# Kernel tuning notes

Hardware: AMD Instinct MI355X
Metric: run time of the kernel (lower is better)

## Reference

```python
import jax, jax.numpy as jnp
import numpy as np

B, N_IN, N_OUT, DEG = 128, 16384, 8192, 64
N_EDGES = N_OUT * DEG


def setup_inputs() -> dict:
    key = jax.random.key(0)
    k_x, k_src, k_dst, k_w = jax.random.split(key, 4)
    x = jax.random.normal(k_x, (B, N_IN), dtype=jnp.float32)
    # Ragged connectivity flattened to a CSR-like edge list:
    # edge_src[e] -> input feature index, edge_dst[e] -> output unit index.
    edge_src = jax.random.randint(k_src, (N_EDGES,), 0, N_IN, dtype=jnp.int64)
    edge_dst = jnp.sort(jax.random.randint(k_dst, (N_EDGES,), 0, N_OUT, dtype=jnp.int64))
    w = jax.random.normal(k_w, (N_EDGES,), dtype=jnp.float32) * 0.05  # one weight per edge
    bias = jnp.zeros((N_OUT,), dtype=jnp.float32)
    return {"x": x, "w": w, "bias": bias, "edge_src": edge_src, "edge_dst": edge_dst}


def reference(x, w, bias, edge_src, edge_dst):
    # Equivalent to: for each output j, y[:, j] = relu(x[:, edges_j] @ w_j + bias[j])
    # Vectorized as a single gather + weighted scatter-add over the flat edge list.
    n_out = bias.shape[0]
    gathered = x[:, edge_src] * w  # [B, E]
    y = jnp.zeros((x.shape[0], n_out), dtype=x.dtype).at[:, edge_dst].add(gathered)
    return jax.nn.relu(y + bias)
```

## Files before the change

### kernel.cpp

```cpp
#include <hip/hip_runtime.h>
#include <hip/hip_fp16.h>

#define B_DIM   128
#define N_IN    16384
#define N_OUT   8192
#define N_EDGES (N_OUT * 64)

#define J_BLK    8
#define THREADS  (J_BLK * 64)
#define JGROUPS  (N_OUT / J_BLK)

__device__ __forceinline__ int lower_bound_dev(const int* __restrict__ a, int n, int v) {
    int lo = 0, hi = n;
    while (lo < hi) {
        int mid = (lo + hi) >> 1;
        if (a[mid] < v) lo = mid + 1; else hi = mid;
    }
    return lo;
}

__global__ void build_rowptr_kernel(const int* __restrict__ dst, int* __restrict__ rp) {
    const int e = blockIdx.x * blockDim.x + threadIdx.x;
    if (e >= N_EDGES) return;
    const int d     = __builtin_nontemporal_load(dst + e);
    const int dprev = (e == 0) ? -1 : __builtin_nontemporal_load(dst + e - 1);
    for (int j = dprev + 1; j <= d; ++j) rp[j] = e;
    if (e == N_EDGES - 1)
        for (int j = d + 1; j <= N_OUT; ++j) rp[j] = N_EDGES;
}

__global__ __launch_bounds__(256) void transpose_h_kernel(const float* __restrict__ x,
                                                          __half* __restrict__ xTh) {
    __shared__ float tile[64][33];
    const int i0 = blockIdx.x * 32;
    const int b0 = blockIdx.y * 64;
    const int tx = threadIdx.x;
    const int ty = threadIdx.y;
#pragma unroll
    for (int r = 0; r < 64; r += 8)
        tile[ty + r][tx] = __builtin_nontemporal_load(&x[(size_t)(b0 + ty + r) * N_IN + (i0 + tx)]);
    __syncthreads();
    __half2* out = (__half2*)xTh;
#pragma unroll
    for (int rr = 0; rr < 4; ++rr) {
        const int il = rr * 8 + ty;
        const float a = tile[2 * tx][il];
        const float b = tile[2 * tx + 1][il];
        out[(size_t)(i0 + il) * (B_DIM / 2) + (b0 >> 1) + tx] = __floats2half2_rn(a, b);
    }
}

__global__ __launch_bounds__(THREADS, 8) void sparse_layer_h(
        const __half* __restrict__ xTh, const float* __restrict__ w,
        const float* __restrict__ bias, const int* __restrict__ src,
        const int* __restrict__ rp, float* __restrict__ y) {
    __shared__ float tile[J_BLK][132];

    const int tid  = threadIdx.x;
    const int wid  = tid >> 6;
    const int lane = tid & 63;
    const int slot = lane >> 4;
    const int bl   = lane & 15;
    const int j0   = blockIdx.x * J_BLK;
    const int j    = j0 + wid;

    const int e0 = __builtin_amdgcn_readfirstlane(rp[j]);
    const int e1 = __builtin_amdgcn_readfirstlane(rp[j + 1]);

    float acc[8] = {0.f, 0.f, 0.f, 0.f, 0.f, 0.f, 0.f, 0.f};
    const char* xbase = (const char*)xTh + bl * 16;

#pragma unroll 4
    for (int e = e0; e < e1; e += 4) {
        const int  ee    = e + slot;
        const bool valid = ee < e1;
        const int  ec    = valid ? ee : e0;
        const int  s     = __builtin_nontemporal_load(src + ec);
        const float wt   = valid ? __builtin_nontemporal_load(w + ec) : 0.f;
        const float4 raw = *(const float4*)(xbase + (size_t)s * (B_DIM * 2));
        const __half2* hp = (const __half2*)&raw;
#pragma unroll
        for (int q = 0; q < 4; ++q) {
            const float2 f = __half22float2(hp[q]);
            acc[2 * q]     = fmaf(f.x, wt, acc[2 * q]);
            acc[2 * q + 1] = fmaf(f.y, wt, acc[2 * q + 1]);
        }
    }

#pragma unroll
    for (int m = 16; m <= 32; m <<= 1)
#pragma unroll
        for (int q = 0; q < 8; ++q) acc[q] += __shfl_xor(acc[q], m, 64);

    if (slot == 0) {
#pragma unroll
        for (int q = 0; q < 8; ++q) tile[wid][8 * bl + q] = acc[q];
    }
    __syncthreads();

#pragma unroll
    for (int i = tid; i < B_DIM * J_BLK; i += THREADS) {
        const int bb = i >> 3;
        const int jj = i & (J_BLK - 1);
        const float v = tile[jj][bb] + bias[j0 + jj];
        __builtin_nontemporal_store(fmaxf(v, 0.f), &y[(size_t)bb * N_OUT + (j0 + jj)]);
    }
}

__global__ __launch_bounds__(THREADS) void sparse_layer_fallback(
        const float* __restrict__ x, const float* __restrict__ w,
        const float* __restrict__ bias, const int* __restrict__ src,
        const int* __restrict__ dst, float* __restrict__ y) {
    __shared__ float tile[J_BLK][130];
    __shared__ int   srp[J_BLK + 1];

    const int tid  = threadIdx.x;
    const int wid  = tid >> 6;
    const int lane = tid & 63;
    const int j0   = blockIdx.x * J_BLK;

    if (tid <= J_BLK) srp[tid] = lower_bound_dev(dst, N_EDGES, j0 + tid);
    __syncthreads();

    const int e0 = srp[wid], e1 = srp[wid + 1];
    const int b0 = lane * 2;
    float acc0 = 0.f, acc1 = 0.f;
    for (int e = e0; e < e1; ++e) {
        const int   s  = src[e];
        const float wt = w[e];
        acc0 = fmaf(x[(size_t)b0 * N_IN + s], wt, acc0);
        acc1 = fmaf(x[(size_t)(b0 + 1) * N_IN + s], wt, acc1);
    }
    tile[wid][b0]     = acc0;
    tile[wid][b0 + 1] = acc1;
    __syncthreads();
#pragma unroll
    for (int i = tid; i < B_DIM * J_BLK; i += THREADS) {
        const int bb = i >> 3;
        const int jj = i & (J_BLK - 1);
        const float v = tile[jj][bb] + bias[j0 + jj];
        y[(size_t)bb * N_OUT + (j0 + jj)] = fmaxf(v, 0.f);
    }
}

extern "C" void kernel_launch(void* const* d_in, const int* in_sizes, int n_in,
                              void* d_out, int out_size, void* d_ws, size_t ws_size,
                              hipStream_t stream) {
    const float* x    = (const float*)d_in[0];
    const float* w    = (const float*)d_in[1];
    const float* bias = (const float*)d_in[2];
    const int*   esrc = (const int*)d_in[3];
    const int*   edst = (const int*)d_in[4];
    float*       y    = (float*)d_out;

    const size_t XT_OFF   = 65536;
    const size_t XT_BYTES = (size_t)N_IN * B_DIM * sizeof(__half);

    const bool has_ws = ws_size >= XT_OFF + XT_BYTES;

    int*    rp  = (int*)d_ws;
    __half* xTh = (__half*)((char*)d_ws + XT_OFF);

    if (has_ws) {
        build_rowptr_kernel<<<(N_EDGES + 255) / 256, 256, 0, stream>>>(edst, rp);
        transpose_h_kernel<<<dim3(N_IN / 32, B_DIM / 64), dim3(32, 8), 0, stream>>>(x, xTh);
        sparse_layer_h<<<dim3(JGROUPS), THREADS, 0, stream>>>(xTh, w, bias, esrc, rp, y);
    } else {
        sparse_layer_fallback<<<dim3(N_OUT / J_BLK), THREADS, 0, stream>>>(x, w, bias, esrc, edst, y);
    }
}
```

Baseline: 90.98 us.

## Split batch into two 64-wide slabs processed by separate sparse-layer passes

```diff
diff --git a/kernel.cpp b/kernel.cpp
--- a/kernel.cpp
+++ b/kernel.cpp
@@ -5,6 +5,9 @@
 #define N_IN    16384
 #define N_OUT   8192
 #define N_EDGES (N_OUT * 64)
+
+#define CHUNKB  64
+#define NPASS   (B_DIM / CHUNKB)
 
 #define J_BLK    8
 #define THREADS  (J_BLK * 64)
@@ -29,38 +32,39 @@
         for (int j = d + 1; j <= N_OUT; ++j) rp[j] = N_EDGES;
 }
 
-__global__ __launch_bounds__(256) void transpose_h_kernel(const float* __restrict__ x,
-                                                          __half* __restrict__ xTh) {
+__global__ __launch_bounds__(256) void transpose_c_kernel(const float* __restrict__ x,
+                                                          __half* __restrict__ xC) {
     __shared__ float tile[64][33];
-    const int i0 = blockIdx.x * 32;
-    const int b0 = blockIdx.y * 64;
-    const int tx = threadIdx.x;
-    const int ty = threadIdx.y;
+    const int i0   = blockIdx.x * 32;
+    const int b0   = blockIdx.y * 64;
+    const int slab = blockIdx.y;
+    const int tx   = threadIdx.x;
+    const int ty   = threadIdx.y;
 #pragma unroll
     for (int r = 0; r < 64; r += 8)
         tile[ty + r][tx] = __builtin_nontemporal_load(&x[(size_t)(b0 + ty + r) * N_IN + (i0 + tx)]);
     __syncthreads();
-    __half2* out = (__half2*)xTh;
+    __half2* out = (__half2*)xC;
 #pragma unroll
     for (int rr = 0; rr < 4; ++rr) {
         const int il = rr * 8 + ty;
         const float a = tile[2 * tx][il];
         const float b = tile[2 * tx + 1][il];
-        out[(size_t)(i0 + il) * (B_DIM / 2) + (b0 >> 1) + tx] = __floats2half2_rn(a, b);
+        out[((size_t)slab * N_IN + (i0 + il)) * (CHUNKB / 2) + tx] = __floats2half2_rn(a, b);
     }
 }
 
-__global__ __launch_bounds__(THREADS, 8) void sparse_layer_h(
-        const __half* __restrict__ xTh, const float* __restrict__ w,
+__global__ __launch_bounds__(THREADS, 8) void sparse_layer_c(
+        const __half* __restrict__ xslab, const float* __restrict__ w,
         const float* __restrict__ bias, const int* __restrict__ src,
-        const int* __restrict__ rp, float* __restrict__ y) {
-    __shared__ float tile[J_BLK][132];
+        const int* __restrict__ rp, float* __restrict__ y, int boff) {
+    __shared__ float tile[J_BLK][68];
 
     const int tid  = threadIdx.x;
     const int wid  = tid >> 6;
     const int lane = tid & 63;
-    const int slot = lane >> 4;
-    const int bl   = lane & 15;
+    const int slot = lane >> 3;
+    const int bl   = lane & 7;
     const int j0   = blockIdx.x * J_BLK;
     const int j    = j0 + wid;
 
@@ -68,16 +72,16 @@
     const int e1 = __builtin_amdgcn_readfirstlane(rp[j + 1]);
 
     float acc[8] = {0.f, 0.f, 0.f, 0.f, 0.f, 0.f, 0.f, 0.f};
-    const char* xbase = (const char*)xTh + bl * 16;
+    const char* xbase = (const char*)xslab + bl * 16;
 
-#pragma unroll 4
-    for (int e = e0; e < e1; e += 4) {
+#pragma unroll 2
+    for (int e = e0; e < e1; e += 8) {
         const int  ee    = e + slot;
         const bool valid = ee < e1;
         const int  ec    = valid ? ee : e0;
         const int  s     = __builtin_nontemporal_load(src + ec);
         const float wt   = valid ? __builtin_nontemporal_load(w + ec) : 0.f;
-        const float4 raw = *(const float4*)(xbase + (size_t)s * (B_DIM * 2));
+        const float4 raw = *(const float4*)(xbase + (size_t)s * (CHUNKB * 2));
         const __half2* hp = (const __half2*)&raw;
 #pragma unroll
         for (int q = 0; q < 4; ++q) {
@@ -88,7 +92,7 @@
     }
 
 #pragma unroll
-    for (int m = 16; m <= 32; m <<= 1)
+    for (int m = 8; m <= 32; m <<= 1)
 #pragma unroll
         for (int q = 0; q < 8; ++q) acc[q] += __shfl_xor(acc[q], m, 64);
 
@@ -98,12 +102,11 @@
     }
     __syncthreads();
 
-#pragma unroll
-    for (int i = tid; i < B_DIM * J_BLK; i += THREADS) {
-        const int bb = i >> 3;
-        const int jj = i & (J_BLK - 1);
+    {
+        const int bb = tid >> 3;
+        const int jj = tid & (J_BLK - 1);
         const float v = tile[jj][bb] + bias[j0 + jj];
-        __builtin_nontemporal_store(fmaxf(v, 0.f), &y[(size_t)bb * N_OUT + (j0 + jj)]);
+        __builtin_nontemporal_store(fmaxf(v, 0.f), &y[(size_t)(boff + bb) * N_OUT + (j0 + jj)]);
     }
 }
 
@@ -154,17 +157,21 @@
     float*       y    = (float*)d_out;
 
     const size_t XT_OFF   = 65536;
-    const size_t XT_BYTES = (size_t)N_IN * B_DIM * sizeof(__half);
+    const size_t XT_BYTES = (size_t)NPASS * N_IN * CHUNKB * sizeof(__half);
 
     const bool has_ws = ws_size >= XT_OFF + XT_BYTES;
 
-    int*    rp  = (int*)d_ws;
-    __half* xTh = (__half*)((char*)d_ws + XT_OFF);
+    int*    rp = (int*)d_ws;
+    __half* xC = (__half*)((char*)d_ws + XT_OFF);
 
     if (has_ws) {
         build_rowptr_kernel<<<(N_EDGES + 255) / 256, 256, 0, stream>>>(edst, rp);
-        transpose_h_kernel<<<dim3(N_IN / 32, B_DIM / 64), dim3(32, 8), 0, stream>>>(x, xTh);
-        sparse_layer_h<<<dim3(JGROUPS), THREADS, 0, stream>>>(xTh, w, bias, esrc, rp, y);
+        transpose_c_kernel<<<dim3(N_IN / 32, NPASS), dim3(32, 8), 0, stream>>>(x, xC);
+        for (int p = 0; p < NPASS; ++p) {
+            const __half* xslab = xC + (size_t)p * N_IN * CHUNKB;
+            sparse_layer_c<<<dim3(JGROUPS), THREADS, 0, stream>>>(
+                xslab, w, bias, esrc, rp, y, p * CHUNKB);
+        }
     } else {
         sparse_layer_fallback<<<dim3(N_OUT / J_BLK), THREADS, 0, stream>>>(x, w, bias, esrc, edst, y);
     }
```

Result: slower. 94.19 us (+3.5%).
